# Kernel tuning notes

Hardware: AMD Instinct MI355X
Metric: run time of the kernel (lower is better)

The kernel has to match this reference:

```python
import jax, jax.numpy as jnp
import numpy as np

B, S, D = 4, 2048, 1024
NH = 16
H2 = NH // 2
F = D // NH  # per-head hidden = 64
EXP = 4
DECAY_CONST = S // 512  # 4
EPS = 1e-5


def setup_inputs() -> dict:
    key = jax.random.key(0)
    ks = jax.random.split(key, 8)
    inp = {
        "x": jax.random.normal(ks[0], (B, S, D), dtype=jnp.float32),
        # token_norm / channel_norm params (LayerNorm init: ones/zeros)
        "g1": jnp.ones((D,), jnp.float32), "b1": jnp.zeros((D,), jnp.float32),
        "g2": jnp.ones((D,), jnp.float32), "b2": jnp.zeros((D,), jnp.float32),
        # per-head input projections [NH, D, F] and output projection
        "Wp": jax.random.normal(ks[1], (NH, D, F), jnp.float32) * 0.02,
        "bp": jnp.zeros((NH, F), jnp.float32),
        "Wo": jax.random.normal(ks[2], (D, D), jnp.float32) * 0.02,
        "bo": jnp.zeros((D,), jnp.float32),
        # ColRepeatCausalLinear: weight = 0.4, bias = 3 ; RowRepeat: -0.3, 0.2
        "w_col": jnp.full((H2, S), 0.4, jnp.float32),
        "b_col": jnp.full((H2, S), 3.0, jnp.float32),
        "w_row": jnp.full((H2, S), -0.3, jnp.float32),
        "b_row": jnp.full((H2, S), 0.2, jnp.float32),
        # decay_value params (ones, clipped to [0.9, 1] then ** (1/decay_constant))
        "dcol": jnp.ones((H2,), jnp.float32),
        "drow": jnp.ones((H2,), jnp.float32),
        # channel MLP
        "W1": jax.random.normal(ks[3], (D, EXP * D), jnp.float32) * 0.02,
        "c1": jnp.zeros((EXP * D,), jnp.float32),
        "W2": jax.random.normal(ks[4], (EXP * D, D), jnp.float32) * 0.02,
        "c2": jnp.zeros((D,), jnp.float32),
    }
    return inp


def _ln(x, g, b):
    m = jnp.mean(x, axis=-1, keepdims=True)
    v = jnp.mean(jnp.square(x - m), axis=-1, keepdims=True)
    return (x - m) * jax.lax.rsqrt(v + EPS) * g + b


def _forward(x, g1, b1, g2, b2, Wp, bp, Wo, bo, w_col, b_col, w_row, b_row,
             dcol, drow, W1, c1, W2, c2):
    decay_c = jnp.clip(dcol, 0.9, 1.0) ** (1.0 / DECAY_CONST)  # [H2]
    decay_r = jnp.clip(drow, 0.9, 1.0) ** (1.0 / DECAY_CONST)  # [H2]

    def step(carry, inp):
        cc, rc = carry                      # each [B, H2, F]
        xt, wc, bc, wr, br = inp            # xt [B, D]; wc/bc/wr/br [H2]
        # token mixing branch
        h = _ln(xt, g1, b1)
        proj = jnp.einsum('bd,hdf->bhf', h, Wp) + bp  # [B, NH, F]
        # Col heads: cache = proj + decay*cache ; out = w*cache + b
        cc = proj[:, :H2] + decay_c[None, :, None] * cc
        col_out = wc[None, :, None] * cc + bc[None, :, None]
        # Row heads: cache = w*proj + decay*cache ; out = cache + b
        rc = wr[None, :, None] * proj[:, H2:] + decay_r[None, :, None] * rc
        row_out = rc + br[None, :, None]
        mix = jnp.concatenate([col_out, row_out], axis=1).reshape(xt.shape[0], -1)
        y = xt + mix @ Wo + bo
        # channel MLP branch
        h2 = _ln(y, g2, b2)
        out = y + jax.nn.gelu(h2 @ W1 + c1) @ W2 + c2
        return (cc, rc), out

    init = (jnp.zeros((x.shape[0], H2, F), x.dtype),
            jnp.zeros((x.shape[0], H2, F), x.dtype))
    xs = (jnp.swapaxes(x, 0, 1), w_col.T, b_col.T, w_row.T, b_row.T)
    _, ys = jax.lax.scan(step, init, xs)    # ys [S, B, D]
    return jnp.swapaxes(ys, 0, 1)


def reference(x, g1, b1, g2, b2, Wp, bp, Wo, bo, w_col, b_col, w_row, b_row,
              dcol, drow, W1, c1, W2, c2):
    return _forward(x, g1, b1, g2, b2, Wp, bp, Wo, bo, w_col, b_col,
                    w_row, b_row, dcol, drow, W1, c1, W2, c2)
```

## Files before the change

kernel.cpp:

```cpp
#include <hip/hip_runtime.h>

typedef __attribute__((ext_vector_type(4))) float fx4;
typedef __attribute__((ext_vector_type(8))) short s16x8;
typedef __attribute__((ext_vector_type(4))) int   i32x4;
typedef __attribute__((ext_vector_type(8))) int   i32x8;

#define SEQ   2048
#define DM    1024
#define BSZ   4
#define ROWS  (BSZ*SEQ)
#define CHUNK 64
#define NCH   (SEQ/CHUNK)

__device__ __forceinline__ unsigned short f2bf(float f){
  unsigned u = __builtin_bit_cast(unsigned, f);
  u = u + 0x7FFFu + ((u >> 16) & 1u);
  return (unsigned short)(u >> 16);
}
__device__ __forceinline__ float bf2f(unsigned short u){
  return __builtin_bit_cast(float, ((unsigned)u) << 16);
}

__device__ __forceinline__ unsigned char f2fp8(float x){
  unsigned u = __builtin_bit_cast(unsigned, x);
  unsigned s = (u >> 24) & 0x80u;
  float ax = __builtin_fabsf(x);
  if (ax >= 448.f) return (unsigned char)(s | 0x7Eu);
  if (ax < 0.015625f){
    int m = (int)(ax * 512.f + 0.5f);
    return (unsigned char)(s | (unsigned)m);
  }
  unsigned b = __builtin_bit_cast(unsigned, ax);
  b += 0x0007FFFFu + ((b >> 20) & 1u);
  unsigned e = (b >> 23) - 127u + 7u;
  unsigned m = (b >> 20) & 7u;
  return (unsigned char)(s | (e << 3) | m);
}

__device__ __forceinline__ float gelu_f(float x){
  float u = 0.7978845608028654f * (x + 0.044715f * x*x*x);
  return x / (1.0f + __expf(-2.0f*u));
}

__device__ __forceinline__ void gload_lds16(const void* g, void* l){
  __builtin_amdgcn_global_load_lds(
      (__attribute__((address_space(1))) void*)g,
      (__attribute__((address_space(3))) void*)l, 16, 0, 0);
}

__device__ __forceinline__ fx4 mfma_mx(i32x8 a, i32x8 b, fx4 c){
  return __builtin_amdgcn_mfma_scale_f32_16x16x128_f8f6f4(
      a, b, c, 0 , 0 ,
      0, 0x7F7F7F7F, 0, 0x79797979);
}

__global__ __launch_bounds__(256) void transpose_k(const float* __restrict__ in,
    unsigned short* __restrict__ out, int R, int C, long long ibs, long long obs){
  __shared__ float tile[32][33];
  in  += (long long)blockIdx.z * ibs;
  out += (long long)blockIdx.z * obs;
  int c0 = blockIdx.x*32, r0 = blockIdx.y*32;
  int tx = threadIdx.x, ty = threadIdx.y;
  #pragma unroll
  for (int i=0;i<4;i++)
    tile[ty+8*i][tx] = in[(long long)(r0+ty+8*i)*C + c0+tx];
  __syncthreads();
  #pragma unroll
  for (int i=0;i<4;i++)
    out[(long long)(c0+ty+8*i)*R + r0+tx] = f2bf(tile[tx][ty+8*i]);
}

__global__ __launch_bounds__(256) void transpose_f8(const float* __restrict__ in,
    unsigned char* __restrict__ out, int R, int C){
  __shared__ float tile[32][33];
  int c0 = blockIdx.x*32, r0 = blockIdx.y*32;
  int tx = threadIdx.x, ty = threadIdx.y;
  #pragma unroll
  for (int i=0;i<4;i++)
    tile[ty+8*i][tx] = in[(long long)(r0+ty+8*i)*C + c0+tx];
  __syncthreads();
  #pragma unroll
  for (int i=0;i<4;i++)
    out[(long long)(c0+ty+8*i)*R + r0+tx] = f2fp8(tile[tx][ty+8*i] * 64.f);
}

__global__ __launch_bounds__(256) void ln_rows(const float* __restrict__ x,
    const float* __restrict__ g, const float* __restrict__ b,
    unsigned short* __restrict__ out){
  int row = blockIdx.x, t = threadIdx.x;
  const fx4* xr = (const fx4*)(x + (long long)row*DM);
  fx4 v = xr[t];
  float s  = v[0]+v[1]+v[2]+v[3];
  float s2 = v[0]*v[0]+v[1]*v[1]+v[2]*v[2]+v[3]*v[3];
  #pragma unroll
  for (int o=32;o;o>>=1){ s += __shfl_down(s,o); s2 += __shfl_down(s2,o); }
  __shared__ float red[8];
  int lane = t & 63, wid = t >> 6;
  if (lane==0){ red[wid]=s; red[4+wid]=s2; }
  __syncthreads();
  s  = red[0]+red[1]+red[2]+red[3];
  s2 = red[4]+red[5]+red[6]+red[7];
  float m  = s * (1.0f/DM);
  float rs = rsqrtf(s2*(1.0f/DM) - m*m + 1e-5f);
  const fx4 gv = ((const fx4*)g)[t], bv = ((const fx4*)b)[t];
  ushort4 pk;
  pk.x = f2bf((v[0]-m)*rs*gv[0] + bv[0]);
  pk.y = f2bf((v[1]-m)*rs*gv[1] + bv[1]);
  pk.z = f2bf((v[2]-m)*rs*gv[2] + bv[2]);
  pk.w = f2bf((v[3]-m)*rs*gv[3] + bv[3]);
  *(ushort4*)(out + (long long)row*DM + t*4) = pk;
}

__global__ __launch_bounds__(256) void ln_rows_f8(const float* __restrict__ x,
    const float* __restrict__ g, const float* __restrict__ b,
    unsigned char* __restrict__ out){
  int row = blockIdx.x, t = threadIdx.x;
  const fx4* xr = (const fx4*)(x + (long long)row*DM);
  fx4 v = xr[t];
  float s  = v[0]+v[1]+v[2]+v[3];
  float s2 = v[0]*v[0]+v[1]*v[1]+v[2]*v[2]+v[3]*v[3];
  #pragma unroll
  for (int o=32;o;o>>=1){ s += __shfl_down(s,o); s2 += __shfl_down(s2,o); }
  __shared__ float red[8];
  int lane = t & 63, wid = t >> 6;
  if (lane==0){ red[wid]=s; red[4+wid]=s2; }
  __syncthreads();
  s  = red[0]+red[1]+red[2]+red[3];
  s2 = red[4]+red[5]+red[6]+red[7];
  float m  = s * (1.0f/DM);
  float rs = rsqrtf(s2*(1.0f/DM) - m*m + 1e-5f);
  const fx4 gv = ((const fx4*)g)[t], bv = ((const fx4*)b)[t];
  uchar4 pk;
  pk.x = f2fp8((v[0]-m)*rs*gv[0] + bv[0]);
  pk.y = f2fp8((v[1]-m)*rs*gv[1] + bv[1]);
  pk.z = f2fp8((v[2]-m)*rs*gv[2] + bv[2]);
  pk.w = f2fp8((v[3]-m)*rs*gv[3] + bv[3]);
  *(uchar4*)(out + (long long)row*DM + t*4) = pk;
}

__global__ __launch_bounds__(256) void scan_carry(const unsigned short* __restrict__ P,
    const float* __restrict__ w_row, const float* __restrict__ dcol,
    const float* __restrict__ drow, float* __restrict__ carry){
  int g = blockIdx.x*4 + (threadIdx.x>>6);
  int lane = threadIdx.x & 63;
  int chunk = g & (NCH-1); int bh = g >> 5; int h = bh & 15; int b = bh >> 4;
  float draw = (h<8) ? dcol[h] : drow[h-8];
  float d = powf(fminf(fmaxf(draw,0.9f),1.0f), 0.25f);
  float c = 0.f;
  const unsigned short* p = P + ((long long)(b*SEQ + chunk*CHUNK))*DM + h*64 + lane;
  const float* wr = w_row + (h>=8 ? (h-8)*SEQ + chunk*CHUNK : 0);
  #pragma unroll 4
  for (int i=0;i<CHUNK;i++){
    float a = bf2f(p[(long long)i*DM]);
    if (h>=8) a *= wr[i];
    c = fmaf(d, c, a);
  }
  carry[((long long)(bh*64 + lane))*NCH + chunk] = c;
}

__global__ __launch_bounds__(256) void scan_final(const unsigned short* __restrict__ P,
    const float* __restrict__ w_col, const float* __restrict__ b_col,
    const float* __restrict__ w_row, const float* __restrict__ b_row,
    const float* __restrict__ dcol, const float* __restrict__ drow,
    const float* __restrict__ carry, unsigned short* __restrict__ mix){
  int g = blockIdx.x*4 + (threadIdx.x>>6);
  int lane = threadIdx.x & 63;
  int chunk = g & (NCH-1); int bh = g >> 5; int h = bh & 15; int b = bh >> 4;
  float draw = (h<8) ? dcol[h] : drow[h-8];
  float d = powf(fminf(fmaxf(draw,0.9f),1.0f), 0.25f);
  float dL = d;
  #pragma unroll
  for (int i=0;i<6;i++) dL *= dL;
  const float* cr = carry + ((long long)(bh*64 + lane))*NCH;
  float c = 0.f;
  for (int j=0;j<chunk;j++) c = fmaf(dL, c, cr[j]);
  const unsigned short* p = P + ((long long)(b*SEQ + chunk*CHUNK))*DM + h*64 + lane;
  unsigned short* mo = mix + ((long long)(b*SEQ + chunk*CHUNK))*DM + h*64 + lane;
  int t0 = chunk*CHUNK;
  #pragma unroll 4
  for (int i=0;i<CHUNK;i++){
    int t = t0 + i;
    float a = bf2f(p[(long long)i*DM]);
    float o;
    if (h<8){
      c = fmaf(d, c, a);
      o = w_col[h*SEQ + t]*c + b_col[h*SEQ + t];
    } else {
      a *= w_row[(h-8)*SEQ + t];
      c = fmaf(d, c, a);
      o = c + b_row[(h-8)*SEQ + t];
    }
    mo[(long long)i*DM] = f2bf(o);
  }
}

template<int EPI, int K>
__global__ __launch_bounds__(256) void gemm_bt(const unsigned short* __restrict__ A,
    const unsigned short* __restrict__ Bt, int N,
    const float* __restrict__ bias, const float* __restrict__ res,
    float* __restrict__ outf, unsigned short* __restrict__ outb){
  __shared__ __align__(16) unsigned short lds[32768];
  const int tid = threadIdx.x;
  const int l = tid & 63;
  const int w = tid >> 6;
  const int wr = w >> 1, wc = w & 1;
  const long long row0 = (long long)blockIdx.x * 128;
  const long long col0 = (long long)blockIdx.y * 128;

  fx4 acc[4][4] = {};

  const unsigned short* gA[4];
  const unsigned short* gB[4];
  int lslot[4];
  #pragma unroll
  for (int i=0;i<4;i++){
    int slot = w*256 + i*64 + l;
    int r = slot >> 3;
    int qs = slot & 7;
    int c = (qs ^ (r & 7)) << 3;
    gA[i] = A  + (row0 + r)*(long long)K + c;
    gB[i] = Bt + (col0 + r)*(long long)K + c;
    lslot[i] = slot*8;
  }
  int aoff[2][4], boff[2][4];
  #pragma unroll
  for (int kk=0;kk<2;kk++){
    #pragma unroll
    for (int m=0;m<4;m++){
      int r  = wr*64 + m*16 + (l&15);
      int q  = (kk*4 + (l>>4)) ^ (r&7);
      aoff[kk][m] = r*64 + q*8;
      int r2 = wc*64 + m*16 + (l&15);
      int q2 = (kk*4 + (l>>4)) ^ (r2&7);
      boff[kk][m] = 8192 + r2*64 + q2*8;
    }
  }
  auto STAGE = [&](int bufoff){
    #pragma unroll
    for (int i=0;i<4;i++){
      gload_lds16(gA[i], &lds[bufoff + lslot[i]]);
      gload_lds16(gB[i], &lds[bufoff + 8192 + lslot[i]]);
      gA[i] += 64; gB[i] += 64;
    }
  };
  constexpr int nsteps = K >> 6;
  STAGE(0);
  STAGE(16384);
  asm volatile("s_waitcnt vmcnt(8)" ::: "memory");
  __builtin_amdgcn_sched_barrier(0);
  __builtin_amdgcn_s_barrier();

  int curoff = 0;
  for (int s = 0; s < nsteps; ++s){
    s16x8 af[2][4], bfr[2][4];
    #pragma unroll
    for (int kk=0;kk<2;kk++){
      #pragma unroll
      for (int m=0;m<4;m++){
        af[kk][m]  = *(const s16x8*)&lds[curoff + aoff[kk][m]];
        bfr[kk][m] = *(const s16x8*)&lds[curoff + boff[kk][m]];
      }
    }
    __builtin_amdgcn_sched_barrier(0);
    asm volatile("s_waitcnt lgkmcnt(0)" ::: "memory");
    __builtin_amdgcn_sched_barrier(0);
    __builtin_amdgcn_s_barrier();
    __builtin_amdgcn_sched_barrier(0);
    const bool do_stage = (s + 2 < nsteps);
    if (do_stage) STAGE(curoff);
    __builtin_amdgcn_s_setprio(1);
    #pragma unroll
    for (int kk=0;kk<2;kk++)
      #pragma unroll
      for (int m=0;m<4;m++)
        #pragma unroll
        for (int n=0;n<4;n++)
          acc[m][n] = __builtin_amdgcn_mfma_f32_16x16x32_bf16(af[kk][m], bfr[kk][n], acc[m][n], 0, 0, 0);
    __builtin_amdgcn_s_setprio(0);
    if (s + 1 < nsteps){
      __builtin_amdgcn_sched_barrier(0);
      if (do_stage) asm volatile("s_waitcnt vmcnt(8)" ::: "memory");
      else          asm volatile("s_waitcnt vmcnt(0)" ::: "memory");
      __builtin_amdgcn_sched_barrier(0);
      __builtin_amdgcn_s_barrier();
      __builtin_amdgcn_sched_barrier(0);
    }
    curoff ^= 16384;
  }
  __syncthreads();

  float* lf = (float*)lds;
  const int lg = l >> 4, lc = l & 15;
  #pragma unroll
  for (int g=0; g<4; ++g){
    if (wr == (g>>1)){
      #pragma unroll
      for (int mm=0; mm<2; ++mm){
        const int m = (g&1)*2 + mm;
        int lrow = mm*16 + lg*4;
        #pragma unroll
        for (int n=0;n<4;n++){
          int col = wc*64 + n*16 + lc;
          #pragma unroll
          for (int rg=0;rg<4;rg++)
            lf[(lrow+rg)*132 + col] = acc[m][n][rg];
        }
      }
    }
    __syncthreads();
    #pragma unroll
    for (int j=0;j<4;j++){
      int flat = j*256 + tid;
      int lrow = flat >> 5, c4 = flat & 31;
      long long grow = row0 + g*32 + lrow;
      long long gcol = col0 + c4*4;
      fx4 v = *(fx4*)&lf[lrow*132 + c4*4];
      fx4 bv = *(const fx4*)&bias[gcol];
      v = v + bv;
      long long idx = grow*(long long)N + gcol;
      if constexpr (EPI==0){
        *(fx4*)&outf[idx] = v;
      } else if constexpr (EPI==1){
        fx4 rv = *(const fx4*)&res[idx];
        v = v + rv;
        *(fx4*)&outf[idx] = v;
      } else {
        ushort4 pk;
        pk.x = f2bf(v[0]); pk.y = f2bf(v[1]);
        pk.z = f2bf(v[2]); pk.w = f2bf(v[3]);
        *(ushort4*)&outb[idx] = pk;
      }
    }
    __syncthreads();
  }
}

template<int EPI, int K>
__global__ __launch_bounds__(256) void gemm_f8(const unsigned char* __restrict__ A,
    const unsigned char* __restrict__ Bt, int N,
    const float* __restrict__ bias, const float* __restrict__ res,
    float* __restrict__ outf, unsigned char* __restrict__ outb){
  __shared__ __align__(16) unsigned char lds[65536];
  const int tid = threadIdx.x;
  const int l = tid & 63;
  const int w = tid >> 6;
  const int wr = w >> 1, wc = w & 1;
  const long long row0 = (long long)blockIdx.x * 128;
  const long long col0 = (long long)blockIdx.y * 128;

  fx4 acc[4][4] = {};

  const unsigned char* gA[4];
  const unsigned char* gB[4];
  int lslot[4];
  #pragma unroll
  for (int i=0;i<4;i++){
    int slot = w*256 + i*64 + l;
    int r = slot >> 3;
    int qs = slot & 7;
    int c = (qs ^ (r & 7)) << 4;
    gA[i] = A  + (row0 + r)*(long long)K + c;
    gB[i] = Bt + (col0 + r)*(long long)K + c;
    lslot[i] = slot*16;
  }
  int aoff0[4], aoff1[4], boff0[4], boff1[4];
  const int lg = l >> 4, l15 = l & 15;
  #pragma unroll
  for (int m=0;m<4;m++){
    int r  = wr*64 + m*16 + l15;
    aoff0[m] = r*128 + ((2*lg  ) ^ (r&7))*16;
    aoff1[m] = r*128 + ((2*lg+1) ^ (r&7))*16;
    int r2 = wc*64 + m*16 + l15;
    boff0[m] = 16384 + r2*128 + ((2*lg  ) ^ (r2&7))*16;
    boff1[m] = 16384 + r2*128 + ((2*lg+1) ^ (r2&7))*16;
  }
  auto STAGE = [&](int bufoff){
    #pragma unroll
    for (int i=0;i<4;i++){
      gload_lds16(gA[i], &lds[bufoff + lslot[i]]);
      gload_lds16(gB[i], &lds[bufoff + 16384 + lslot[i]]);
      gA[i] += 128; gB[i] += 128;
    }
  };
  constexpr int nsteps = K >> 7;
  STAGE(0);
  STAGE(32768);
  asm volatile("s_waitcnt vmcnt(8)" ::: "memory");
  __builtin_amdgcn_sched_barrier(0);
  __builtin_amdgcn_s_barrier();

  int curoff = 0;
  for (int s = 0; s < nsteps; ++s){
    i32x8 av[4], bv[4];
    #pragma unroll
    for (int m=0;m<4;m++){
      i32x4 lo = *(const i32x4*)&lds[curoff + aoff0[m]];
      i32x4 hi = *(const i32x4*)&lds[curoff + aoff1[m]];
      av[m][0]=lo[0]; av[m][1]=lo[1]; av[m][2]=lo[2]; av[m][3]=lo[3];
      av[m][4]=hi[0]; av[m][5]=hi[1]; av[m][6]=hi[2]; av[m][7]=hi[3];
    }
    #pragma unroll
    for (int n=0;n<4;n++){
      i32x4 lo = *(const i32x4*)&lds[curoff + boff0[n]];
      i32x4 hi = *(const i32x4*)&lds[curoff + boff1[n]];
      bv[n][0]=lo[0]; bv[n][1]=lo[1]; bv[n][2]=lo[2]; bv[n][3]=lo[3];
      bv[n][4]=hi[0]; bv[n][5]=hi[1]; bv[n][6]=hi[2]; bv[n][7]=hi[3];
    }
    __builtin_amdgcn_sched_barrier(0);
    asm volatile("s_waitcnt lgkmcnt(0)" ::: "memory");
    __builtin_amdgcn_sched_barrier(0);
    __builtin_amdgcn_s_barrier();
    __builtin_amdgcn_sched_barrier(0);
    const bool do_stage = (s + 2 < nsteps);
    if (do_stage) STAGE(curoff);
    __builtin_amdgcn_s_setprio(1);
    #pragma unroll
    for (int m=0;m<4;m++)
      #pragma unroll
      for (int n=0;n<4;n++)
        acc[m][n] = mfma_mx(av[m], bv[n], acc[m][n]);
    __builtin_amdgcn_s_setprio(0);
    if (s + 1 < nsteps){
      __builtin_amdgcn_sched_barrier(0);
      if (do_stage) asm volatile("s_waitcnt vmcnt(8)" ::: "memory");
      else          asm volatile("s_waitcnt vmcnt(0)" ::: "memory");
      __builtin_amdgcn_sched_barrier(0);
      __builtin_amdgcn_s_barrier();
      __builtin_amdgcn_sched_barrier(0);
    }
    curoff ^= 32768;
  }
  __syncthreads();

  float* lf = (float*)lds;
  #pragma unroll
  for (int g=0; g<4; ++g){
    if (wr == (g>>1)){
      #pragma unroll
      for (int mm=0; mm<2; ++mm){
        const int m = (g&1)*2 + mm;
        int lrow = mm*16 + lg*4;
        #pragma unroll
        for (int n=0;n<4;n++){
          int col = wc*64 + n*16 + l15;
          #pragma unroll
          for (int rg=0;rg<4;rg++)
            lf[(lrow+rg)*132 + col] = acc[m][n][rg];
        }
      }
    }
    __syncthreads();
    #pragma unroll
    for (int j=0;j<4;j++){
      int flat = j*256 + tid;
      int lrow = flat >> 5, c4 = flat & 31;
      long long grow = row0 + g*32 + lrow;
      long long gcol = col0 + c4*4;
      fx4 v = *(fx4*)&lf[lrow*132 + c4*4];
      fx4 bv2 = *(const fx4*)&bias[gcol];
      v = v + bv2;
      long long idx = grow*(long long)N + gcol;
      if constexpr (EPI==1){
        fx4 rv = *(const fx4*)&res[idx];
        v = v + rv;
        *(fx4*)&outf[idx] = v;
      } else {
        uchar4 pk;
        pk.x = f2fp8(gelu_f(v[0]));
        pk.y = f2fp8(gelu_f(v[1]));
        pk.z = f2fp8(gelu_f(v[2]));
        pk.w = f2fp8(gelu_f(v[3]));
        *(uchar4*)&outb[idx] = pk;
      }
    }
    __syncthreads();
  }
}

extern "C" void kernel_launch(void* const* d_in, const int* in_sizes, int n_in,
                              void* d_out, int out_size, void* d_ws, size_t ws_size,
                              hipStream_t stream){
  const float* x    = (const float*)d_in[0];
  const float* g1   = (const float*)d_in[1];
  const float* b1   = (const float*)d_in[2];
  const float* g2   = (const float*)d_in[3];
  const float* b2   = (const float*)d_in[4];
  const float* Wp   = (const float*)d_in[5];
  const float* bp   = (const float*)d_in[6];
  const float* Wo   = (const float*)d_in[7];
  const float* bo   = (const float*)d_in[8];
  const float* w_col= (const float*)d_in[9];
  const float* b_col= (const float*)d_in[10];
  const float* w_row= (const float*)d_in[11];
  const float* b_row= (const float*)d_in[12];
  const float* dcol = (const float*)d_in[13];
  const float* drow = (const float*)d_in[14];
  const float* W1   = (const float*)d_in[15];
  const float* c1   = (const float*)d_in[16];
  const float* W2   = (const float*)d_in[17];
  const float* c2   = (const float*)d_in[18];
  float* out = (float*)d_out;

  char* ws = (char*)d_ws;
  const size_t MB = 1024*1024;
  if (ws_size < 101*MB) return;
  unsigned short* Wpt  = (unsigned short*)(ws + 0);
  unsigned short* Wot  = (unsigned short*)(ws + 2*MB);
  unsigned char*  W1t8 = (unsigned char*)(ws + 4*MB);
  unsigned char*  W2t8 = (unsigned char*)(ws + 12*MB);
  unsigned short* h    = (unsigned short*)(ws + 20*MB);
  unsigned char*  yln8 = (unsigned char*)(ws + 20*MB);
  unsigned short* P    = (unsigned short*)(ws + 36*MB);
  unsigned char*  U8   = (unsigned char*)(ws + 36*MB);
  unsigned short* mix  = (unsigned short*)(ws + 68*MB);
  float*          carry= (float*)(ws + 84*MB);

  dim3 tb(32,8);
  transpose_k <<<dim3(2,32,16),  tb, 0, stream>>>(Wp, Wpt, 1024,   64, 65536LL, 65536LL);
  transpose_k <<<dim3(32,32,1),  tb, 0, stream>>>(Wo, Wot, 1024, 1024, 0LL, 0LL);
  transpose_f8<<<dim3(128,32,1), tb, 0, stream>>>(W1, W1t8, 1024, 4096);
  transpose_f8<<<dim3(32,128,1), tb, 0, stream>>>(W2, W2t8, 4096, 1024);

  ln_rows<<<dim3(ROWS), dim3(256), 0, stream>>>(x, g1, b1, h);
  gemm_bt<3,1024><<<dim3(64,8),  dim3(256), 0, stream>>>(h,   Wpt, 1024, bp, nullptr, nullptr, P);
  scan_carry<<<dim3(512), dim3(256), 0, stream>>>(P, w_row, dcol, drow, carry);
  scan_final<<<dim3(512), dim3(256), 0, stream>>>(P, w_col, b_col, w_row, b_row, dcol, drow, carry, mix);
  gemm_bt<1,1024><<<dim3(64,8),  dim3(256), 0, stream>>>(mix, Wot, 1024, bo, x, out, nullptr);
  ln_rows_f8<<<dim3(ROWS), dim3(256), 0, stream>>>(out, g2, b2, yln8);
  gemm_f8<2,1024><<<dim3(64,32), dim3(256), 0, stream>>>(yln8, W1t8, 4096, c1, nullptr, nullptr, U8);
  gemm_f8<1,4096><<<dim3(64,8),  dim3(256), 0, stream>>>(U8,  W2t8, 1024, c2, out, out, nullptr);
}
```

Measured before the change: 311.4 us.

## Simplify FP8 GEMM main loop to single-ahead prefetch with full barriers

Replaces the two-deep global-to-LDS prefetch, which used hand-placed vmcnt/lgkmcnt waits and split barriers, with a simpler scheme. Each iteration now stages the next K tile into the other buffer, computes from the current one, and ends with __syncthreads. The per-lane K-slice LDS offsets change to lg and 4+lg 16-byte chunks, applied the same way to A and B so the dot product is unchanged. A fragments are now loaded per m inside the MFMA loop to reduce live registers. The cost is that prefetch depth drops to one tile and every full barrier waits for all outstanding loads, so less load latency may be hidden.

```diff
diff --git a/kernel.cpp b/kernel.cpp
--- a/kernel.cpp
+++ b/kernel.cpp
@@ -363,16 +363,16 @@
     gB[i] = Bt + (col0 + r)*(long long)K + c;
     lslot[i] = slot*16;
   }
-  int aoff0[4], aoff1[4], boff0[4], boff1[4];
   const int lg = l >> 4, l15 = l & 15;
+  int aoffL[4], aoffH[4], boffL[4], boffH[4];
   #pragma unroll
   for (int m=0;m<4;m++){
     int r  = wr*64 + m*16 + l15;
-    aoff0[m] = r*128 + ((2*lg  ) ^ (r&7))*16;
-    aoff1[m] = r*128 + ((2*lg+1) ^ (r&7))*16;
+    aoffL[m] = r*128 + ((lg  ) ^ (r&7))*16;
+    aoffH[m] = r*128 + ((4+lg) ^ (r&7))*16;
     int r2 = wc*64 + m*16 + l15;
-    boff0[m] = 16384 + r2*128 + ((2*lg  ) ^ (r2&7))*16;
-    boff1[m] = 16384 + r2*128 + ((2*lg+1) ^ (r2&7))*16;
+    boffL[m] = 16384 + r2*128 + ((lg  ) ^ (r2&7))*16;
+    boffH[m] = 16384 + r2*128 + ((4+lg) ^ (r2&7))*16;
   }
   auto STAGE = [&](int bufoff){
     #pragma unroll
@@ -384,53 +384,32 @@
   };
   constexpr int nsteps = K >> 7;
   STAGE(0);
-  STAGE(32768);
-  asm volatile("s_waitcnt vmcnt(8)" ::: "memory");
-  __builtin_amdgcn_sched_barrier(0);
-  __builtin_amdgcn_s_barrier();
+  __syncthreads();
 
   int curoff = 0;
   for (int s = 0; s < nsteps; ++s){
-    i32x8 av[4], bv[4];
+    if (s + 1 < nsteps) STAGE(curoff ^ 32768);
+    i32x8 bv[4];
+    #pragma unroll
+    for (int n=0;n<4;n++){
+      i32x4 lo = *(const i32x4*)&lds[curoff + boffL[n]];
+      i32x4 hi = *(const i32x4*)&lds[curoff + boffH[n]];
+      bv[n] = __builtin_shufflevector(lo, hi, 0,1,2,3,4,5,6,7);
+    }
+    __builtin_amdgcn_s_setprio(1);
     #pragma unroll
     for (int m=0;m<4;m++){
-      i32x4 lo = *(const i32x4*)&lds[curoff + aoff0[m]];
-      i32x4 hi = *(const i32x4*)&lds[curoff + aoff1[m]];
-      av[m][0]=lo[0]; av[m][1]=lo[1]; av[m][2]=lo[2]; av[m][3]=lo[3];
-      av[m][4]=hi[0]; av[m][5]=hi[1]; av[m][6]=hi[2]; av[m][7]=hi[3];
-    }
-    #pragma unroll
-    for (int n=0;n<4;n++){
-      i32x4 lo = *(const i32x4*)&lds[curoff + boff0[n]];
-      i32x4 hi = *(const i32x4*)&lds[curoff + boff1[n]];
-      bv[n][0]=lo[0]; bv[n][1]=lo[1]; bv[n][2]=lo[2]; bv[n][3]=lo[3];
-      bv[n][4]=hi[0]; bv[n][5]=hi[1]; bv[n][6]=hi[2]; bv[n][7]=hi[3];
-    }
-    __builtin_amdgcn_sched_barrier(0);
-    asm volatile("s_waitcnt lgkmcnt(0)" ::: "memory");
-    __builtin_amdgcn_sched_barrier(0);
-    __builtin_amdgcn_s_barrier();
-    __builtin_amdgcn_sched_barrier(0);
-    const bool do_stage = (s + 2 < nsteps);
-    if (do_stage) STAGE(curoff);
-    __builtin_amdgcn_s_setprio(1);
-    #pragma unroll
-    for (int m=0;m<4;m++)
+      i32x4 lo = *(const i32x4*)&lds[curoff + aoffL[m]];
+      i32x4 hi = *(const i32x4*)&lds[curoff + aoffH[m]];
+      i32x8 av = __builtin_shufflevector(lo, hi, 0,1,2,3,4,5,6,7);
       #pragma unroll
       for (int n=0;n<4;n++)
-        acc[m][n] = mfma_mx(av[m], bv[n], acc[m][n]);
+        acc[m][n] = mfma_mx(av, bv[n], acc[m][n]);
+    }
     __builtin_amdgcn_s_setprio(0);
-    if (s + 1 < nsteps){
-      __builtin_amdgcn_sched_barrier(0);
-      if (do_stage) asm volatile("s_waitcnt vmcnt(8)" ::: "memory");
-      else          asm volatile("s_waitcnt vmcnt(0)" ::: "memory");
-      __builtin_amdgcn_sched_barrier(0);
-      __builtin_amdgcn_s_barrier();
-      __builtin_amdgcn_sched_barrier(0);
-    }
+    __syncthreads();
     curoff ^= 32768;
   }
-  __syncthreads();
 
   float* lf = (float*)lds;
   #pragma unroll
```

Measured after the change: 308.8 us. Within noise of the previous version (-0.8%).
